# Kernel optimization log

Hardware: AMD Instinct MI355X
Metric: run time of the kernel (lower is better)

The kernel has to match this reference:

```python
import jax, jax.numpy as jnp
import numpy as np

K, OUT, IN = 4, 4096, 4096
B, S = 2, 2048

def setup_inputs() -> dict:
    key = jax.random.key(0)
    k1, k2, k3 = jax.random.split(key, 3)
    x = jax.random.normal(k1, (B, S, IN), dtype=jnp.float32)
    alphas = jax.random.normal(k2, (K,), dtype=jnp.float32)
    # binary bases in {-1, +1}, stored as int8 like the torch buffer
    bases = (jax.random.randint(k3, (K, OUT, IN), 0, 2) * 2 - 1).astype(jnp.int8)
    return {"x": x, "alphas": alphas, "bases": bases}

def reference(x, alphas, bases):
    # W_q = sum_i alphas[i] * bases[i]  -> [out, in]
    W_q = jnp.einsum('k,koi->oi', alphas, bases.astype(x.dtype))
    # y = x @ W_q.T  -> [B, S, out]
    return jnp.einsum('bsi,oi->bso', x, W_q)
```

## Files before the change

kernel.cpp:

```cpp
#include <hip/hip_runtime.h>
#include <hip/hip_bf16.h>
#include <stdint.h>

#define DIM_M 4096
#define DIM_N 4096
#define DIM_K 4096
#define BASE_STRIDE (DIM_N * DIM_K)
#define NT (DIM_K / 64)

typedef __bf16 bf16x8 __attribute__((ext_vector_type(8)));
typedef float floatx4 __attribute__((ext_vector_type(4)));
typedef unsigned short ushort8 __attribute__((ext_vector_type(8)));

__device__ __forceinline__ unsigned short f2bf(float f) {
    uint32_t u = __float_as_uint(f);
    uint32_t r = (u + 0x7FFFu + ((u >> 16) & 1u)) >> 16;
    return (unsigned short)r;
}

__global__ __launch_bounds__(256) void prep_kernel(
        const int* __restrict__ bases, const float* __restrict__ alphas,
        const float* __restrict__ x,
        unsigned short* __restrict__ Wb, unsigned short* __restrict__ Xb) {
    const int bid = blockIdx.x;
    if (bid < 8192) {
        const long e = ((long)bid * 256 + threadIdx.x) * 8;
        const float a0 = alphas[0], a1 = alphas[1], a2 = alphas[2], a3 = alphas[3];
        const int4 p0 = *(const int4*)(bases + e);
        const int4 p1 = *(const int4*)(bases + e + 4);
        const int4 q0 = *(const int4*)(bases + BASE_STRIDE + e);
        const int4 q1 = *(const int4*)(bases + BASE_STRIDE + e + 4);
        const int4 r0 = *(const int4*)(bases + 2L * BASE_STRIDE + e);
        const int4 r1 = *(const int4*)(bases + 2L * BASE_STRIDE + e + 4);
        const int4 s0 = *(const int4*)(bases + 3L * BASE_STRIDE + e);
        const int4 s1 = *(const int4*)(bases + 3L * BASE_STRIDE + e + 4);
        ushort8 o;
        o[0] = f2bf(a0 * p0.x + a1 * q0.x + a2 * r0.x + a3 * s0.x);
        o[1] = f2bf(a0 * p0.y + a1 * q0.y + a2 * r0.y + a3 * s0.y);
        o[2] = f2bf(a0 * p0.z + a1 * q0.z + a2 * r0.z + a3 * s0.z);
        o[3] = f2bf(a0 * p0.w + a1 * q0.w + a2 * r0.w + a3 * s0.w);
        o[4] = f2bf(a0 * p1.x + a1 * q1.x + a2 * r1.x + a3 * s1.x);
        o[5] = f2bf(a0 * p1.y + a1 * q1.y + a2 * r1.y + a3 * s1.y);
        o[6] = f2bf(a0 * p1.z + a1 * q1.z + a2 * r1.z + a3 * s1.z);
        o[7] = f2bf(a0 * p1.w + a1 * q1.w + a2 * r1.w + a3 * s1.w);
        *(ushort8*)(Wb + e) = o;
    } else {
        const long e = ((long)(bid - 8192) * 256 + threadIdx.x) * 8;
        const float4 v0 = *(const float4*)(x + e);
        const float4 v1 = *(const float4*)(x + e + 4);
        ushort8 o;
        o[0] = f2bf(v0.x); o[1] = f2bf(v0.y); o[2] = f2bf(v0.z); o[3] = f2bf(v0.w);
        o[4] = f2bf(v1.x); o[5] = f2bf(v1.y); o[6] = f2bf(v1.z); o[7] = f2bf(v1.w);
        *(ushort8*)(Xb + e) = o;
    }
}

#define MFMA16 __builtin_amdgcn_mfma_f32_16x16x32_bf16
#define BAR()   __builtin_amdgcn_s_barrier()
#define PRIO1() __builtin_amdgcn_s_setprio(1)
#define PRIO0() __builtin_amdgcn_s_setprio(0)

__device__ __forceinline__ void stage_half(const unsigned short* __restrict__ gb,
        int grow0, int kbase, unsigned short* ld, int wave, int lane) {
#pragma unroll
    for (int r = 0; r < 2; ++r) {
        const int row = wave * 16 + r * 8 + (lane >> 3);
        const int ch  = (lane & 7) ^ (row & 7);
        const unsigned short* g = gb + (size_t)(grow0 + row) * DIM_K + kbase + ch * 8;
        unsigned short* d = ld + (wave * 16 + r * 8) * 64;
        __builtin_amdgcn_global_load_lds(
            (const __attribute__((address_space(1))) unsigned int*)((const void*)g),
            (__attribute__((address_space(3))) unsigned int*)((void*)d), 16, 0, 0);
    }
}

#define DS_A16(LD, MF, SLOT)                                                          \
    do {                                                                              \
        aR[SLOT][0] = *(const bf16x8*)((LD) + ((MF) * 16 + l15) * 64 + cko2[0]);      \
        aR[SLOT][1] = *(const bf16x8*)((LD) + ((MF) * 16 + l15) * 64 + cko2[1]);      \
    } while (0)
#define DS_B16(LD, NF, SLOT)                                                          \
    do {                                                                              \
        bR[SLOT][0] = *(const bf16x8*)((LD) + (nloc + (NF) * 16 + l15) * 64 + cko2[0]); \
        bR[SLOT][1] = *(const bf16x8*)((LD) + (nloc + (NF) * 16 + l15) * 64 + cko2[1]); \
    } while (0)
#define MMQ(MB, NB)                                                                   \
    do { _Pragma("unroll") for (int kh = 0; kh < 2; ++kh)                             \
        _Pragma("unroll") for (int n = 0; n < 2; ++n)                                 \
            _Pragma("unroll") for (int m = 0; m < 4; ++m)                             \
                acc4[(MB) + m][(NB) + n] = MFMA16(aR[m][kh], bR[(NB) + n][kh],        \
                                                  acc4[(MB) + m][(NB) + n], 0, 0, 0); \
    } while (0)

__global__ __launch_bounds__(512, 2) void gemm_bt_kernel(
        const unsigned short* __restrict__ A, const unsigned short* __restrict__ Bt,
        float* __restrict__ C) {
    __shared__ __align__(16) unsigned short lds[2][2][2][128 * 64];

    const int t = threadIdx.x;
    const int wave = t >> 6, lane = t & 63;
    const int l15 = lane & 15, l4 = lane >> 4;
    const int wm = wave >> 2;
    const int wn = wave & 3;
    const int nloc = (wn & 1) * 64;

    const int mBase = blockIdx.y * 256;
    const int nBase = blockIdx.x * 256;

    const unsigned short* LA0 = &lds[0][0][wm][0];
    const unsigned short* LA1 = &lds[1][0][wm][0];
    const unsigned short* LB0 = &lds[0][1][wn >> 1][0];
    const unsigned short* LB1 = &lds[1][1][wn >> 1][0];

    int cko2[2];
#pragma unroll
    for (int kh = 0; kh < 2; ++kh) cko2[kh] = ((l4 + 4 * kh) ^ (l15 & 7)) * 8;

    floatx4 acc4[8][4] = {};
    bf16x8 aR[4][2], bR[4][2];

    stage_half(A,  mBase + 0,   0,  &lds[0][0][0][0], wave, lane);
    stage_half(A,  mBase + 128, 0,  &lds[0][0][1][0], wave, lane);
    stage_half(Bt, nBase + 0,   0,  &lds[0][1][0][0], wave, lane);
    stage_half(Bt, nBase + 128, 0,  &lds[0][1][1][0], wave, lane);
    stage_half(Bt, nBase + 0,   64, &lds[1][1][0][0], wave, lane);
    stage_half(Bt, nBase + 128, 64, &lds[1][1][1][0], wave, lane);
    stage_half(A,  mBase + 0,   64, &lds[1][0][0][0], wave, lane);
    asm volatile("s_waitcnt vmcnt(6)" ::: "memory");
    BAR();

    for (int i = 0; i < NT / 2; ++i) {
        const bool more = (i < NT / 2 - 1);
        const int t1k = (2 * i + 1) * 64;
        const int t2k = (2 * i + 2) * 64;
        const int t3k = (2 * i + 3) * 64;

        DS_A16(LA0, 0, 0); DS_A16(LA0, 1, 1); DS_A16(LA0, 2, 2); DS_A16(LA0, 3, 3);
        DS_B16(LB0, 0, 0); DS_B16(LB0, 1, 1);
        stage_half(A, mBase + 128, t1k, &lds[1][0][1][0], wave, lane);
        BAR(); PRIO1(); MMQ(0, 0); PRIO0(); BAR();
        DS_B16(LB0, 2, 2); DS_B16(LB0, 3, 3);
        BAR(); PRIO1(); MMQ(0, 2); PRIO0(); BAR();
        DS_A16(LA0, 4, 0); DS_A16(LA0, 5, 1); DS_A16(LA0, 6, 2); DS_A16(LA0, 7, 3);
        if (more) stage_half(Bt, nBase + 0, t2k, &lds[0][1][0][0], wave, lane);
        BAR(); PRIO1(); MMQ(4, 2); PRIO0(); BAR();
        if (more) {
            stage_half(Bt, nBase + 128, t2k, &lds[0][1][1][0], wave, lane);
            stage_half(A,  mBase + 0,   t2k, &lds[0][0][0][0], wave, lane);
            asm volatile("s_waitcnt vmcnt(6)" ::: "memory");
        } else {
            asm volatile("s_waitcnt vmcnt(0)" ::: "memory");
        }
        BAR(); PRIO1(); MMQ(4, 0); PRIO0(); BAR();

        DS_A16(LA1, 0, 0); DS_A16(LA1, 1, 1); DS_A16(LA1, 2, 2); DS_A16(LA1, 3, 3);
        DS_B16(LB1, 0, 0); DS_B16(LB1, 1, 1);
        if (more) stage_half(A, mBase + 128, t2k, &lds[0][0][1][0], wave, lane);
        BAR(); PRIO1(); MMQ(0, 0); PRIO0(); BAR();
        DS_B16(LB1, 2, 2); DS_B16(LB1, 3, 3);
        BAR(); PRIO1(); MMQ(0, 2); PRIO0(); BAR();
        DS_A16(LA1, 4, 0); DS_A16(LA1, 5, 1); DS_A16(LA1, 6, 2); DS_A16(LA1, 7, 3);
        if (more) stage_half(Bt, nBase + 0, t3k, &lds[1][1][0][0], wave, lane);
        BAR(); PRIO1(); MMQ(4, 2); PRIO0(); BAR();
        if (more) {
            stage_half(Bt, nBase + 128, t3k, &lds[1][1][1][0], wave, lane);
            stage_half(A,  mBase + 0,   t3k, &lds[1][0][0][0], wave, lane);
            asm volatile("s_waitcnt vmcnt(6)" ::: "memory");
        } else {
            asm volatile("s_waitcnt vmcnt(0)" ::: "memory");
        }
        BAR(); PRIO1(); MMQ(4, 0); PRIO0(); BAR();
    }

#pragma unroll
    for (int mf = 0; mf < 8; ++mf) {
#pragma unroll
        for (int nf = 0; nf < 4; ++nf) {
#pragma unroll
            for (int r = 0; r < 4; ++r) {
                const int row = mBase + wm * 128 + mf * 16 + l4 * 4 + r;
                const int col = nBase + wn * 64 + nf * 16 + l15;
                C[(size_t)row * DIM_N + col] = acc4[mf][nf][r];
            }
        }
    }
}

__global__ __launch_bounds__(256) void naive_kernel(
        const float* __restrict__ x, const float* __restrict__ alphas,
        const int* __restrict__ bases, float* __restrict__ out) {
    const long o = (long)blockIdx.x * 256 + threadIdx.x;
    const int m = (int)(o >> 12), n = (int)(o & 4095);
    const float a0 = alphas[0], a1 = alphas[1], a2 = alphas[2], a3 = alphas[3];
    const float* xr = x + (long)m * DIM_K;
    const int* b0 = bases + (long)n * DIM_K;
    const int* b1 = b0 + BASE_STRIDE;
    const int* b2 = b1 + BASE_STRIDE;
    const int* b3 = b2 + BASE_STRIDE;
    float acc = 0.f;
    for (int i = 0; i < DIM_K; i++) {
        float w = a0 * b0[i] + a1 * b1[i] + a2 * b2[i] + a3 * b3[i];
        acc += xr[i] * w;
    }
    out[o] = acc;
}

extern "C" void kernel_launch(void* const* d_in, const int* in_sizes, int n_in,
                              void* d_out, int out_size, void* d_ws, size_t ws_size,
                              hipStream_t stream) {
    const float* x      = (const float*)d_in[0];
    const float* alphas = (const float*)d_in[1];
    const int*   bases  = (const int*)d_in[2];
    float* out = (float*)d_out;

    const size_t need = (size_t)2 * DIM_N * DIM_K + (size_t)2 * DIM_M * DIM_K;
    if (ws_size >= need) {
        unsigned short* Wb = (unsigned short*)d_ws;
        unsigned short* Xb = (unsigned short*)d_ws + (size_t)DIM_N * DIM_K;
        prep_kernel<<<16384, 256, 0, stream>>>(bases, alphas, x, Wb, Xb);
        gemm_bt_kernel<<<dim3(DIM_N / 256, DIM_M / 256), 512, 0, stream>>>(Xb, Wb, out);
    } else {
        naive_kernel<<<(DIM_M * DIM_N) / 256, 256, 0, stream>>>(x, alphas, bases, out);
    }
}
```

Measured before the change: 530.9 us.

## Software-pipeline LDS fragment reads with MFMA and halve barrier count

Moves the LDS fragment loads for the next MFMA quarter so they are issued alongside the current quarter's MFMAs. The first fragments are prefetched before the loop and the next tile's are loaded at the end of each iteration. Each compute step now has one barrier instead of a pair, and LDS read latency is meant to hide behind matrix math. This relies on the register fragment slots not being overwritten while still in use, and on the barrier placement still protecting the LDS buffers from being restaged too early.

```diff
diff --git a/kernel.cpp b/kernel.cpp
--- a/kernel.cpp
+++ b/kernel.cpp
@@ -128,6 +128,8 @@
     stage_half(A,  mBase + 0,   64, &lds[1][0][0][0], wave, lane);
     asm volatile("s_waitcnt vmcnt(6)" ::: "memory");
     BAR();
+    DS_A16(LA0, 0, 0); DS_A16(LA0, 1, 1); DS_A16(LA0, 2, 2); DS_A16(LA0, 3, 3);
+    DS_B16(LB0, 0, 0); DS_B16(LB0, 1, 1);
 
     for (int i = 0; i < NT / 2; ++i) {
         const bool more = (i < NT / 2 - 1);
@@ -135,15 +137,16 @@
         const int t2k = (2 * i + 2) * 64;
         const int t3k = (2 * i + 3) * 64;
 
-        DS_A16(LA0, 0, 0); DS_A16(LA0, 1, 1); DS_A16(LA0, 2, 2); DS_A16(LA0, 3, 3);
-        DS_B16(LB0, 0, 0); DS_B16(LB0, 1, 1);
+        DS_B16(LB0, 2, 2); DS_B16(LB0, 3, 3);
         stage_half(A, mBase + 128, t1k, &lds[1][0][1][0], wave, lane);
-        BAR(); PRIO1(); MMQ(0, 0); PRIO0(); BAR();
-        DS_B16(LB0, 2, 2); DS_B16(LB0, 3, 3);
-        BAR(); PRIO1(); MMQ(0, 2); PRIO0(); BAR();
+        PRIO1(); MMQ(0, 0); PRIO0();
+        BAR();
+        PRIO1(); MMQ(0, 2); PRIO0();
         DS_A16(LA0, 4, 0); DS_A16(LA0, 5, 1); DS_A16(LA0, 6, 2); DS_A16(LA0, 7, 3);
+        BAR();
         if (more) stage_half(Bt, nBase + 0, t2k, &lds[0][1][0][0], wave, lane);
-        BAR(); PRIO1(); MMQ(4, 2); PRIO0(); BAR();
+        PRIO1(); MMQ(4, 2); PRIO0();
+        BAR();
         if (more) {
             stage_half(Bt, nBase + 128, t2k, &lds[0][1][1][0], wave, lane);
             stage_half(A,  mBase + 0,   t2k, &lds[0][0][0][0], wave, lane);
@@ -151,17 +154,22 @@
         } else {
             asm volatile("s_waitcnt vmcnt(0)" ::: "memory");
         }
-        BAR(); PRIO1(); MMQ(4, 0); PRIO0(); BAR();
-
+        BAR();
+        PRIO1(); MMQ(4, 0); PRIO0();
         DS_A16(LA1, 0, 0); DS_A16(LA1, 1, 1); DS_A16(LA1, 2, 2); DS_A16(LA1, 3, 3);
         DS_B16(LB1, 0, 0); DS_B16(LB1, 1, 1);
+        BAR();
+
+        DS_B16(LB1, 2, 2); DS_B16(LB1, 3, 3);
         if (more) stage_half(A, mBase + 128, t2k, &lds[0][0][1][0], wave, lane);
-        BAR(); PRIO1(); MMQ(0, 0); PRIO0(); BAR();
-        DS_B16(LB1, 2, 2); DS_B16(LB1, 3, 3);
-        BAR(); PRIO1(); MMQ(0, 2); PRIO0(); BAR();
+        PRIO1(); MMQ(0, 0); PRIO0();
+        BAR();
+        PRIO1(); MMQ(0, 2); PRIO0();
         DS_A16(LA1, 4, 0); DS_A16(LA1, 5, 1); DS_A16(LA1, 6, 2); DS_A16(LA1, 7, 3);
+        BAR();
         if (more) stage_half(Bt, nBase + 0, t3k, &lds[1][1][0][0], wave, lane);
-        BAR(); PRIO1(); MMQ(4, 2); PRIO0(); BAR();
+        PRIO1(); MMQ(4, 2); PRIO0();
+        BAR();
         if (more) {
             stage_half(Bt, nBase + 128, t3k, &lds[1][1][1][0], wave, lane);
             stage_half(A,  mBase + 0,   t3k, &lds[1][0][0][0], wave, lane);
@@ -169,7 +177,13 @@
         } else {
             asm volatile("s_waitcnt vmcnt(0)" ::: "memory");
         }
-        BAR(); PRIO1(); MMQ(4, 0); PRIO0(); BAR();
+        BAR();
+        PRIO1(); MMQ(4, 0); PRIO0();
+        if (more) {
+            DS_A16(LA0, 0, 0); DS_A16(LA0, 1, 1); DS_A16(LA0, 2, 2); DS_A16(LA0, 3, 3);
+            DS_B16(LB0, 0, 0); DS_B16(LB0, 1, 1);
+        }
+        BAR();
     }
 
 #pragma unroll
```

New measurement: 529.1 us. Within noise of the previous version (-0.3%).
